# Kernel tuning notes

Measured on AMD Instinct MI355X. Metric: run time of the kernel, lower is better.

The kernel has to match this reference:

```python
import jax, jax.numpy as jnp
import numpy as np

B, C, L = 8192, 1, 4096
SCALES = 5
OUT_DIM = 512
STD_FACTOR = 1.0
SQRT_HALF = 0.7071067811865476  # Haar filter coefficient 1/sqrt(2)


def setup_inputs() -> dict:
    key = jax.random.key(0)
    k1, k2 = jax.random.split(key)
    x = jax.random.normal(k1, (B, C, L), dtype=jnp.float32)
    # kaiming_uniform_(a=0): bound = sqrt(2) * sqrt(3 / fan_in)
    fan_in = L  # in_dim_wave == in_dim for dyadic Haar
    bound = np.sqrt(2.0) * np.sqrt(3.0 / fan_in)
    block_mat = jax.random.uniform(k2, (L, OUT_DIM), dtype=jnp.float32,
                                   minval=-bound, maxval=bound)
    return {"x": x, "block_mat": block_mat}


def haar_analysis(x, scales):
    """Multi-level Haar DWT over last axis. Returns [cA_n, cD_n, ..., cD_1]."""
    details = []
    cur = x
    for _ in range(scales):
        even, odd = cur[..., ::2], cur[..., 1::2]
        details.append((even - odd) * SQRT_HALF)  # highpass
        cur = (even + odd) * SQRT_HALF            # lowpass
    return [cur] + details[::-1]


def reference(x, block_mat):
    coeffs = haar_analysis(x, SCALES)
    x_freq_cat = jnp.concatenate(coeffs, axis=-1)        # [B, C, L]
    c_no = x_freq_cat.shape[-1]
    x_freq_mat = x_freq_cat.reshape(-1, c_no)            # [B*C, L]
    a = jnp.abs(x_freq_mat)
    # torch.std is unbiased (ddof=1)
    threshold = jnp.mean(a) + jnp.std(a, ddof=1) * STD_FACTOR
    mask = a > threshold
    # sparse.mm(sparse(masked x), W) == (x * mask) @ W
    x_sparse = jnp.where(mask, x_freq_mat, jnp.zeros((), x_freq_mat.dtype))
    out = jax.nn.relu(x_sparse @ block_mat)              # [B*C, OUT_DIM]
    return out.reshape(x_freq_cat.shape[:-1] + (OUT_DIM,))
```

## Files before the change

kernel.cpp:

```cpp
#include <hip/hip_runtime.h>
#include <hip/hip_bf16.h>
#include <math.h>

#define LDIM 4096
#define NROWS 8192
#define NOUT 512

static const float SQRT_HALF_F = 0.70710678118654752440f;

typedef __attribute__((ext_vector_type(8))) short short8;
typedef __attribute__((ext_vector_type(4))) float f32x4;
typedef __attribute__((ext_vector_type(8))) unsigned short u16x8;
typedef __attribute__((ext_vector_type(4))) unsigned short u16x4;
typedef __attribute__((ext_vector_type(2))) unsigned short u16x2;

#define AM_OFF   0ull
#define WT_OFF   67108864ull
#define PART_OFF (WT_OFF + 4194304ull)
#define THR_OFF  (PART_OFF + 131072ull)

__device__ inline unsigned short f2bf(float f) {
  union { float f; unsigned u; } v; v.f = f;
  unsigned r = (v.u + 0x7fffu + ((v.u >> 16) & 1u)) >> 16;
  return (unsigned short)r;
}

__device__ inline unsigned short mcvt(float f, float thr) {
  return f2bf((fabsf(f) > thr) ? f : 0.0f);
}

__device__ inline void async16(void* l, const void* g) {
  __builtin_amdgcn_global_load_lds((const __attribute__((address_space(1))) void*)g,
                                   (__attribute__((address_space(3))) void*)l, 16, 0, 0);
}

__global__ __launch_bounds__(256) void haar1_kernel(const float* __restrict__ x,
                                                    double* __restrict__ partials,
                                                    const float* __restrict__ W,
                                                    unsigned short* __restrict__ Wt) {
  if (blockIdx.x >= NROWS) {
    __shared__ float tile[32][33];
    const int wb = blockIdx.x - NROWS;
    const int bx = wb & 15;
    const int by = wb >> 4;
    const int tx = threadIdx.x & 31, ty = threadIdx.x >> 5;
#pragma unroll
    for (int j = 0; j < 4; ++j)
      tile[ty + j * 8][tx] = W[(size_t)(by * 32 + ty + j * 8) * NOUT + bx * 32 + tx];
    __syncthreads();
#pragma unroll
    for (int j = 0; j < 4; ++j)
      Wt[(size_t)(bx * 32 + ty + j * 8) * LDIM + by * 32 + tx] = f2bf(tile[tx][ty + j * 8]);
    return;
  }

  __shared__ double red[8];
  const int row = blockIdx.x;
  const int t = threadIdx.x;
  const float S = SQRT_HALF_F;

  const float4* xr = (const float4*)(x + (size_t)row * LDIM) + 4 * t;
  float v[16];
#pragma unroll
  for (int k = 0; k < 4; ++k) {
    float4 q = xr[k];
    v[4 * k] = q.x; v[4 * k + 1] = q.y; v[4 * k + 2] = q.z; v[4 * k + 3] = q.w;
  }

  double sa = 0.0, sq = 0.0;
  float a1[8], a2[4], a3[2], a4;
#pragma unroll
  for (int j = 0; j < 8; ++j) {
    float d = (v[2 * j] - v[2 * j + 1]) * S;
    a1[j] = (v[2 * j] + v[2 * j + 1]) * S;
    sa += (double)fabsf(d); sq += (double)d * (double)d;
  }
#pragma unroll
  for (int j = 0; j < 4; ++j) {
    float d = (a1[2 * j] - a1[2 * j + 1]) * S;
    a2[j] = (a1[2 * j] + a1[2 * j + 1]) * S;
    sa += (double)fabsf(d); sq += (double)d * (double)d;
  }
#pragma unroll
  for (int j = 0; j < 2; ++j) {
    float d = (a2[2 * j] - a2[2 * j + 1]) * S;
    a3[j] = (a2[2 * j] + a2[2 * j + 1]) * S;
    sa += (double)fabsf(d); sq += (double)d * (double)d;
  }
  {
    float d = (a3[0] - a3[1]) * S;
    a4 = (a3[0] + a3[1]) * S;
    sa += (double)fabsf(d); sq += (double)d * (double)d;
  }
  {
    float other = __shfl_xor(a4, 1, 64);
    if ((t & 1) == 0) {
      float d = (a4 - other) * S, ap = (a4 + other) * S;
      sa += (double)fabsf(d) + (double)fabsf(ap);
      sq += (double)d * (double)d + (double)ap * (double)ap;
    }
  }

  const int lane = t & 63, wid = t >> 6;
#pragma unroll
  for (int off = 32; off > 0; off >>= 1) {
    sa += __shfl_down(sa, off, 64);
    sq += __shfl_down(sq, off, 64);
  }
  if (lane == 0) { red[wid] = sa; red[4 + wid] = sq; }
  __syncthreads();
  if (t == 0) {
    partials[2 * (size_t)row + 0] = red[0] + red[1] + red[2] + red[3];
    partials[2 * (size_t)row + 1] = red[4] + red[5] + red[6] + red[7];
  }
}

__global__ __launch_bounds__(1024) void thr_kernel(const double* __restrict__ partials,
                                                   float* __restrict__ thr) {
  __shared__ double red[32];
  const int tid = threadIdx.x;
  double sa = 0.0, sq = 0.0;
#pragma unroll
  for (int k = 0; k < NROWS / 1024; ++k) {
    int i = tid + k * 1024;
    sa += partials[2 * i + 0];
    sq += partials[2 * i + 1];
  }
  const int lane = tid & 63, wid = tid >> 6;
#pragma unroll
  for (int off = 32; off > 0; off >>= 1) {
    sa += __shfl_down(sa, off, 64);
    sq += __shfl_down(sq, off, 64);
  }
  if (lane == 0) { red[wid] = sa; red[16 + wid] = sq; }
  __syncthreads();
  if (tid == 0) {
    double s = 0.0, q = 0.0;
#pragma unroll
    for (int i = 0; i < 16; ++i) { s += red[i]; q += red[16 + i]; }
    const double n = (double)NROWS * (double)LDIM;
    double mean = s / n;
    double var = (q - s * s / n) / (n - 1.0);
    *thr = (float)(mean + sqrt(var));
  }
}

__global__ __launch_bounds__(256) void haar2_kernel(const float* __restrict__ x,
                                                    const float* __restrict__ thrp,
                                                    unsigned short* __restrict__ Am) {
  const float thr = *thrp;
  const int row = blockIdx.x;
  const int t = threadIdx.x;
  const float S = SQRT_HALF_F;

  const float4* xr = (const float4*)(x + (size_t)row * LDIM) + 4 * t;
  float v[16];
#pragma unroll
  for (int k = 0; k < 4; ++k) {
    float4 q = xr[k];
    v[4 * k] = q.x; v[4 * k + 1] = q.y; v[4 * k + 2] = q.z; v[4 * k + 3] = q.w;
  }

  unsigned short* orow = Am + (size_t)row * LDIM;
  float a1[8], a2[4], a3[2], a4;

  u16x8 d1;
#pragma unroll
  for (int j = 0; j < 8; ++j) {
    float d = (v[2 * j] - v[2 * j + 1]) * S;
    a1[j] = (v[2 * j] + v[2 * j + 1]) * S;
    d1[j] = mcvt(d, thr);
  }
  *(u16x8*)(orow + 2048 + 8 * t) = d1;

  u16x4 d2;
#pragma unroll
  for (int j = 0; j < 4; ++j) {
    float d = (a1[2 * j] - a1[2 * j + 1]) * S;
    a2[j] = (a1[2 * j] + a1[2 * j + 1]) * S;
    d2[j] = mcvt(d, thr);
  }
  *(u16x4*)(orow + 1024 + 4 * t) = d2;

  u16x2 d3;
#pragma unroll
  for (int j = 0; j < 2; ++j) {
    float d = (a2[2 * j] - a2[2 * j + 1]) * S;
    a3[j] = (a2[2 * j] + a2[2 * j + 1]) * S;
    d3[j] = mcvt(d, thr);
  }
  *(u16x2*)(orow + 512 + 2 * t) = d3;

  {
    float d = (a3[0] - a3[1]) * S;
    a4 = (a3[0] + a3[1]) * S;
    orow[256 + t] = mcvt(d, thr);
  }
  {
    float other = __shfl_xor(a4, 1, 64);
    if ((t & 1) == 0) {
      float d = (a4 - other) * S, ap = (a4 + other) * S;
      orow[128 + t / 2] = mcvt(d, thr);
      orow[t / 2] = mcvt(ap, thr);
    }
  }
}

__global__ __launch_bounds__(256, 4) void gemm_kernel(const unsigned short* __restrict__ Am,
                                                      const unsigned short* __restrict__ Wt,
                                                      float* __restrict__ out) {
  __shared__ __align__(16) unsigned short As[64 * 128];
  __shared__ __align__(16) unsigned short Bs[64 * 128];

  const int tid = threadIdx.x;
  const int lane = tid & 63, w = tid >> 6;
  const int quad = lane >> 4, l15 = lane & 15;
  const int wm = w >> 1, wn = w & 1;

  const int id = blockIdx.x;
  const int xcd = id & 7, slot = id >> 3;
  const int nblk = slot & 7;
  const int mblk = (slot >> 3) * 8 + xcd;
  const int n0 = nblk * 64, m0 = mblk * 64;

  f32x4 acc[2][2] = {};

  const int rl = lane >> 3;
  const int cg = (lane & 7) ^ rl;
  const unsigned short* AgBase = Am + (size_t)(m0 + rl) * LDIM + cg * 8;
  const unsigned short* BgBase = Wt + (size_t)(n0 + rl) * LDIM + cg * 8;

  for (int k0 = 0; k0 < LDIM; k0 += 128) {
#pragma unroll
    for (int j = 0; j < 2; ++j) {
      const int g = w * 2 + j;
      const size_t gro = (size_t)(g * 8) * LDIM + k0;
      async16(&As[g * 1024], AgBase + gro);
      async16(&As[g * 1024 + 512], AgBase + gro + 64);
      async16(&Bs[g * 1024], BgBase + gro);
      async16(&Bs[g * 1024 + 512], BgBase + gro + 64);
    }
    __syncthreads();

    short8 af[2][4], bf[2][4];
#pragma unroll
    for (int mi = 0; mi < 2; ++mi) {
      const int row = wm * 32 + mi * 16 + l15;
      const int rg = row >> 3, ro = row & 7;
#pragma unroll
      for (int ks = 0; ks < 4; ++ks) {
        const int c = ks * 4 + quad;
        af[mi][ks] = *(const short8*)&As[rg * 1024 + (c & 8) * 64 + ro * 64 + ((c ^ ro) & 7) * 8];
      }
    }
#pragma unroll
    for (int ni = 0; ni < 2; ++ni) {
      const int row = wn * 32 + ni * 16 + l15;
      const int rg = row >> 3, ro = row & 7;
#pragma unroll
      for (int ks = 0; ks < 4; ++ks) {
        const int c = ks * 4 + quad;
        bf[ni][ks] = *(const short8*)&Bs[rg * 1024 + (c & 8) * 64 + ro * 64 + ((c ^ ro) & 7) * 8];
      }
    }
#pragma unroll
    for (int ks = 0; ks < 4; ++ks)
#pragma unroll
      for (int mi = 0; mi < 2; ++mi)
#pragma unroll
        for (int ni = 0; ni < 2; ++ni)
          acc[mi][ni] = __builtin_amdgcn_mfma_f32_16x16x32_bf16(af[mi][ks], bf[ni][ks],
                                                                acc[mi][ni], 0, 0, 0);
    __syncthreads();
  }

#pragma unroll
  for (int mi = 0; mi < 2; ++mi) {
#pragma unroll
    for (int ni = 0; ni < 2; ++ni) {
      const int r0 = m0 + wm * 32 + mi * 16 + quad * 4;
      const int c = n0 + wn * 32 + ni * 16 + l15;
#pragma unroll
      for (int r = 0; r < 4; ++r)
        out[(size_t)(r0 + r) * NOUT + c] = fmaxf(acc[mi][ni][r], 0.0f);
    }
  }
}

extern "C" void kernel_launch(void* const* d_in, const int* in_sizes, int n_in,
                              void* d_out, int out_size, void* d_ws, size_t ws_size,
                              hipStream_t stream) {
  const float* x = (const float*)d_in[0];
  const float* W = (const float*)d_in[1];
  float* out = (float*)d_out;

  char* ws = (char*)d_ws;
  unsigned short* Am = (unsigned short*)(ws + AM_OFF);
  unsigned short* Wt = (unsigned short*)(ws + WT_OFF);
  double* partials = (double*)(ws + PART_OFF);
  float* thr = (float*)(ws + THR_OFF);

  haar1_kernel<<<NROWS + 2048, 256, 0, stream>>>(x, partials, W, Wt);
  thr_kernel<<<1, 1024, 0, stream>>>(partials, thr);
  haar2_kernel<<<NROWS, 256, 0, stream>>>(x, thr, Am);
  gemm_kernel<<<1024, 256, 0, stream>>>(Am, Wt, out);
}
```

Before: 269.1 us.

## Fuse Haar stats, threshold and masking into one cooperative kernel

Measured after the change: 338.3 us. +25.7%, slower.

```diff
diff --git a/kernel.cpp b/kernel.cpp
--- a/kernel.cpp
+++ b/kernel.cpp
@@ -1,10 +1,15 @@
 #include <hip/hip_runtime.h>
 #include <hip/hip_bf16.h>
+#include <hip/hip_cooperative_groups.h>
 #include <math.h>
+
+namespace cg = cooperative_groups;
 
 #define LDIM 4096
 #define NROWS 8192
 #define NOUT 512
+#define CGRID 512
+#define RPB (NROWS / CGRID)
 
 static const float SQRT_HALF_F = 0.70710678118654752440f;
 
@@ -17,7 +22,6 @@
 #define AM_OFF   0ull
 #define WT_OFF   67108864ull
 #define PART_OFF (WT_OFF + 4194304ull)
-#define THR_OFF  (PART_OFF + 131072ull)
 
 __device__ inline unsigned short f2bf(float f) {
   union { float f; unsigned u; } v; v.f = f;
@@ -34,16 +38,85 @@
                                    (__attribute__((address_space(3))) void*)l, 16, 0, 0);
 }
 
-__global__ __launch_bounds__(256) void haar1_kernel(const float* __restrict__ x,
-                                                    double* __restrict__ partials,
-                                                    const float* __restrict__ W,
-                                                    unsigned short* __restrict__ Wt) {
-  if (blockIdx.x >= NROWS) {
-    __shared__ float tile[32][33];
-    const int wb = blockIdx.x - NROWS;
+__global__ __launch_bounds__(256, 2) void haar_all_kernel(const float* __restrict__ x,
+                                                          const float* __restrict__ W,
+                                                          unsigned short* __restrict__ Wt,
+                                                          double* __restrict__ partials,
+                                                          unsigned short* __restrict__ Am) {
+  __shared__ double red[8];
+  __shared__ float tile[32][33];
+  __shared__ float thr_s;
+
+  const int b = blockIdx.x;
+  const int t = threadIdx.x;
+  const int lane = t & 63, wid = t >> 6;
+  const float S = SQRT_HALF_F;
+
+  double tsa = 0.0, tsq = 0.0;
+  for (int rr = 0; rr < RPB; ++rr) {
+    const int row = b * RPB + rr;
+    const float4* xr = (const float4*)(x + (size_t)row * LDIM) + 4 * t;
+    float v[16];
+#pragma unroll
+    for (int k = 0; k < 4; ++k) {
+      float4 q = xr[k];
+      v[4 * k] = q.x; v[4 * k + 1] = q.y; v[4 * k + 2] = q.z; v[4 * k + 3] = q.w;
+    }
+    float a1[8], a2[4], a3[2], a4;
+#pragma unroll
+    for (int j = 0; j < 8; ++j) {
+      float d = (v[2 * j] - v[2 * j + 1]) * S;
+      a1[j] = (v[2 * j] + v[2 * j + 1]) * S;
+      tsa += (double)fabsf(d); tsq += (double)d * (double)d;
+    }
+#pragma unroll
+    for (int j = 0; j < 4; ++j) {
+      float d = (a1[2 * j] - a1[2 * j + 1]) * S;
+      a2[j] = (a1[2 * j] + a1[2 * j + 1]) * S;
+      tsa += (double)fabsf(d); tsq += (double)d * (double)d;
+    }
+#pragma unroll
+    for (int j = 0; j < 2; ++j) {
+      float d = (a2[2 * j] - a2[2 * j + 1]) * S;
+      a3[j] = (a2[2 * j] + a2[2 * j + 1]) * S;
+      tsa += (double)fabsf(d); tsq += (double)d * (double)d;
+    }
+    {
+      float d = (a3[0] - a3[1]) * S;
+      a4 = (a3[0] + a3[1]) * S;
+      tsa += (double)fabsf(d); tsq += (double)d * (double)d;
+    }
+    {
+      float other = __shfl_xor(a4, 1, 64);
+      if ((t & 1) == 0) {
+        float d = (a4 - other) * S, ap = (a4 + other) * S;
+        tsa += (double)fabsf(d) + (double)fabsf(ap);
+        tsq += (double)d * (double)d + (double)ap * (double)ap;
+      }
+    }
+  }
+  {
+    double sa = tsa, sq = tsq;
+#pragma unroll
+    for (int off = 32; off > 0; off >>= 1) {
+      sa += __shfl_down(sa, off, 64);
+      sq += __shfl_down(sq, off, 64);
+    }
+    if (lane == 0) { red[wid] = sa; red[4 + wid] = sq; }
+    __syncthreads();
+    if (t == 0) {
+      partials[2 * (size_t)b + 0] = red[0] + red[1] + red[2] + red[3];
+      partials[2 * (size_t)b + 1] = red[4] + red[5] + red[6] + red[7];
+    }
+  }
+
+  const int tx = t & 31, ty = t >> 5;
+#pragma unroll
+  for (int j4 = 0; j4 < 4; ++j4) {
+    const int wb = b * 4 + j4;
     const int bx = wb & 15;
     const int by = wb >> 4;
-    const int tx = threadIdx.x & 31, ty = threadIdx.x >> 5;
+    __syncthreads();
 #pragma unroll
     for (int j = 0; j < 4; ++j)
       tile[ty + j * 8][tx] = W[(size_t)(by * 32 + ty + j * 8) * NOUT + bx * 32 + tx];
@@ -51,157 +124,86 @@
 #pragma unroll
     for (int j = 0; j < 4; ++j)
       Wt[(size_t)(bx * 32 + ty + j * 8) * LDIM + by * 32 + tx] = f2bf(tile[tx][ty + j * 8]);
-    return;
-  }
-
-  __shared__ double red[8];
-  const int row = blockIdx.x;
-  const int t = threadIdx.x;
-  const float S = SQRT_HALF_F;
-
-  const float4* xr = (const float4*)(x + (size_t)row * LDIM) + 4 * t;
-  float v[16];
-#pragma unroll
-  for (int k = 0; k < 4; ++k) {
-    float4 q = xr[k];
-    v[4 * k] = q.x; v[4 * k + 1] = q.y; v[4 * k + 2] = q.z; v[4 * k + 3] = q.w;
-  }
-
-  double sa = 0.0, sq = 0.0;
-  float a1[8], a2[4], a3[2], a4;
-#pragma unroll
-  for (int j = 0; j < 8; ++j) {
-    float d = (v[2 * j] - v[2 * j + 1]) * S;
-    a1[j] = (v[2 * j] + v[2 * j + 1]) * S;
-    sa += (double)fabsf(d); sq += (double)d * (double)d;
-  }
-#pragma unroll
-  for (int j = 0; j < 4; ++j) {
-    float d = (a1[2 * j] - a1[2 * j + 1]) * S;
-    a2[j] = (a1[2 * j] + a1[2 * j + 1]) * S;
-    sa += (double)fabsf(d); sq += (double)d * (double)d;
-  }
-#pragma unroll
-  for (int j = 0; j < 2; ++j) {
-    float d = (a2[2 * j] - a2[2 * j + 1]) * S;
-    a3[j] = (a2[2 * j] + a2[2 * j + 1]) * S;
-    sa += (double)fabsf(d); sq += (double)d * (double)d;
-  }
+  }
+
+  cg::this_grid().sync();
+
   {
-    float d = (a3[0] - a3[1]) * S;
-    a4 = (a3[0] + a3[1]) * S;
-    sa += (double)fabsf(d); sq += (double)d * (double)d;
-  }
-  {
-    float other = __shfl_xor(a4, 1, 64);
-    if ((t & 1) == 0) {
-      float d = (a4 - other) * S, ap = (a4 + other) * S;
-      sa += (double)fabsf(d) + (double)fabsf(ap);
-      sq += (double)d * (double)d + (double)ap * (double)ap;
-    }
-  }
-
-  const int lane = t & 63, wid = t >> 6;
-#pragma unroll
-  for (int off = 32; off > 0; off >>= 1) {
-    sa += __shfl_down(sa, off, 64);
-    sq += __shfl_down(sq, off, 64);
-  }
-  if (lane == 0) { red[wid] = sa; red[4 + wid] = sq; }
-  __syncthreads();
-  if (t == 0) {
-    partials[2 * (size_t)row + 0] = red[0] + red[1] + red[2] + red[3];
-    partials[2 * (size_t)row + 1] = red[4] + red[5] + red[6] + red[7];
-  }
-}
-
-__global__ __launch_bounds__(1024) void thr_kernel(const double* __restrict__ partials,
-                                                   float* __restrict__ thr) {
-  __shared__ double red[32];
-  const int tid = threadIdx.x;
-  double sa = 0.0, sq = 0.0;
-#pragma unroll
-  for (int k = 0; k < NROWS / 1024; ++k) {
-    int i = tid + k * 1024;
-    sa += partials[2 * i + 0];
-    sq += partials[2 * i + 1];
-  }
-  const int lane = tid & 63, wid = tid >> 6;
-#pragma unroll
-  for (int off = 32; off > 0; off >>= 1) {
-    sa += __shfl_down(sa, off, 64);
-    sq += __shfl_down(sq, off, 64);
-  }
-  if (lane == 0) { red[wid] = sa; red[16 + wid] = sq; }
-  __syncthreads();
-  if (tid == 0) {
-    double s = 0.0, q = 0.0;
-#pragma unroll
-    for (int i = 0; i < 16; ++i) { s += red[i]; q += red[16 + i]; }
-    const double n = (double)NROWS * (double)LDIM;
-    double mean = s / n;
-    double var = (q - s * s / n) / (n - 1.0);
-    *thr = (float)(mean + sqrt(var));
-  }
-}
-
-__global__ __launch_bounds__(256) void haar2_kernel(const float* __restrict__ x,
-                                                    const float* __restrict__ thrp,
-                                                    unsigned short* __restrict__ Am) {
-  const float thr = *thrp;
-  const int row = blockIdx.x;
-  const int t = threadIdx.x;
-  const float S = SQRT_HALF_F;
-
-  const float4* xr = (const float4*)(x + (size_t)row * LDIM) + 4 * t;
-  float v[16];
-#pragma unroll
-  for (int k = 0; k < 4; ++k) {
-    float4 q = xr[k];
-    v[4 * k] = q.x; v[4 * k + 1] = q.y; v[4 * k + 2] = q.z; v[4 * k + 3] = q.w;
-  }
-
-  unsigned short* orow = Am + (size_t)row * LDIM;
-  float a1[8], a2[4], a3[2], a4;
-
-  u16x8 d1;
-#pragma unroll
-  for (int j = 0; j < 8; ++j) {
-    float d = (v[2 * j] - v[2 * j + 1]) * S;
-    a1[j] = (v[2 * j] + v[2 * j + 1]) * S;
-    d1[j] = mcvt(d, thr);
-  }
-  *(u16x8*)(orow + 2048 + 8 * t) = d1;
-
-  u16x4 d2;
-#pragma unroll
-  for (int j = 0; j < 4; ++j) {
-    float d = (a1[2 * j] - a1[2 * j + 1]) * S;
-    a2[j] = (a1[2 * j] + a1[2 * j + 1]) * S;
-    d2[j] = mcvt(d, thr);
-  }
-  *(u16x4*)(orow + 1024 + 4 * t) = d2;
-
-  u16x2 d3;
-#pragma unroll
-  for (int j = 0; j < 2; ++j) {
-    float d = (a2[2 * j] - a2[2 * j + 1]) * S;
-    a3[j] = (a2[2 * j] + a2[2 * j + 1]) * S;
-    d3[j] = mcvt(d, thr);
-  }
-  *(u16x2*)(orow + 512 + 2 * t) = d3;
-
-  {
-    float d = (a3[0] - a3[1]) * S;
-    a4 = (a3[0] + a3[1]) * S;
-    orow[256 + t] = mcvt(d, thr);
-  }
-  {
-    float other = __shfl_xor(a4, 1, 64);
-    if ((t & 1) == 0) {
-      float d = (a4 - other) * S, ap = (a4 + other) * S;
-      orow[128 + t / 2] = mcvt(d, thr);
-      orow[t / 2] = mcvt(ap, thr);
+    double sa = 0.0, sq = 0.0;
+    for (int i = t; i < CGRID; i += 256) {
+      sa += partials[2 * i + 0];
+      sq += partials[2 * i + 1];
+    }
+#pragma unroll
+    for (int off = 32; off > 0; off >>= 1) {
+      sa += __shfl_down(sa, off, 64);
+      sq += __shfl_down(sq, off, 64);
+    }
+    if (lane == 0) { red[wid] = sa; red[4 + wid] = sq; }
+    __syncthreads();
+    if (t == 0) {
+      double s = red[0] + red[1] + red[2] + red[3];
+      double q = red[4] + red[5] + red[6] + red[7];
+      const double n = (double)NROWS * (double)LDIM;
+      double mean = s / n;
+      double var = (q - s * s / n) / (n - 1.0);
+      thr_s = (float)(mean + sqrt(var));
+    }
+    __syncthreads();
+  }
+  const float thr = thr_s;
+
+  for (int rr = 0; rr < RPB; ++rr) {
+    const int row = b * RPB + rr;
+    const float4* xr = (const float4*)(x + (size_t)row * LDIM) + 4 * t;
+    float v[16];
+#pragma unroll
+    for (int k = 0; k < 4; ++k) {
+      float4 q = xr[k];
+      v[4 * k] = q.x; v[4 * k + 1] = q.y; v[4 * k + 2] = q.z; v[4 * k + 3] = q.w;
+    }
+    unsigned short* orow = Am + (size_t)row * LDIM;
+    float a1[8], a2[4], a3[2], a4;
+
+    u16x8 d1;
+#pragma unroll
+    for (int j = 0; j < 8; ++j) {
+      float d = (v[2 * j] - v[2 * j + 1]) * S;
+      a1[j] = (v[2 * j] + v[2 * j + 1]) * S;
+      d1[j] = mcvt(d, thr);
+    }
+    *(u16x8*)(orow + 2048 + 8 * t) = d1;
+
+    u16x4 d2;
+#pragma unroll
+    for (int j = 0; j < 4; ++j) {
+      float d = (a1[2 * j] - a1[2 * j + 1]) * S;
+      a2[j] = (a1[2 * j] + a1[2 * j + 1]) * S;
+      d2[j] = mcvt(d, thr);
+    }
+    *(u16x4*)(orow + 1024 + 4 * t) = d2;
+
+    u16x2 d3;
+#pragma unroll
+    for (int j = 0; j < 2; ++j) {
+      float d = (a2[2 * j] - a2[2 * j + 1]) * S;
+      a3[j] = (a2[2 * j] + a2[2 * j + 1]) * S;
+      d3[j] = mcvt(d, thr);
+    }
+    *(u16x2*)(orow + 512 + 2 * t) = d3;
+
+    {
+      float d = (a3[0] - a3[1]) * S;
+      a4 = (a3[0] + a3[1]) * S;
+      orow[256 + t] = mcvt(d, thr);
+    }
+    {
+      float other = __shfl_xor(a4, 1, 64);
+      if ((t & 1) == 0) {
+        float d = (a4 - other) * S, ap = (a4 + other) * S;
+        orow[128 + t / 2] = mcvt(d, thr);
+        orow[t / 2] = mcvt(ap, thr);
+      }
     }
   }
 }
@@ -226,9 +228,9 @@
   f32x4 acc[2][2] = {};
 
   const int rl = lane >> 3;
-  const int cg = (lane & 7) ^ rl;
-  const unsigned short* AgBase = Am + (size_t)(m0 + rl) * LDIM + cg * 8;
-  const unsigned short* BgBase = Wt + (size_t)(n0 + rl) * LDIM + cg * 8;
+  const int cg_ = (lane & 7) ^ rl;
+  const unsigned short* AgBase = Am + (size_t)(m0 + rl) * LDIM + cg_ * 8;
+  const unsigned short* BgBase = Wt + (size_t)(n0 + rl) * LDIM + cg_ * 8;
 
   for (int k0 = 0; k0 < LDIM; k0 += 128) {
 #pragma unroll
@@ -298,10 +300,9 @@
   unsigned short* Am = (unsigned short*)(ws + AM_OFF);
   unsigned short* Wt = (unsigned short*)(ws + WT_OFF);
   double* partials = (double*)(ws + PART_OFF);
-  float* thr = (float*)(ws + THR_OFF);
-
-  haar1_kernel<<<NROWS + 2048, 256, 0, stream>>>(x, partials, W, Wt);
-  thr_kernel<<<1, 1024, 0, stream>>>(partials, thr);
-  haar2_kernel<<<NROWS, 256, 0, stream>>>(x, thr, Am);
+
+  void* args[] = {(void*)&x, (void*)&W, (void*)&Wt, (void*)&partials, (void*)&Am};
+  hipLaunchCooperativeKernel((const void*)haar_all_kernel, dim3(CGRID), dim3(256),
+                             args, 0, stream);
   gemm_kernel<<<1024, 256, 0, stream>>>(Am, Wt, out);
 }
```
